# Kernel optimization log

Measured on AMD Instinct MI355X. Metric: run time of the kernel, lower is better.

The kernel has to match this reference:

```python
import jax, jax.numpy as jnp
import numpy as np

C = 64
CR = C // 16  # reduction=16 -> query/key channels
B, H, W = 2, 80, 80


def setup_inputs() -> dict:
    key = jax.random.key(0)
    ks = jax.random.split(key, 13)
    s = 0.05
    return {
        "a": jax.random.normal(ks[0], (B, C, H, W), jnp.float32),
        "b": jax.random.normal(ks[1], (B, C, H, W), jnp.float32),
        "c": jax.random.normal(ks[2], (B, C, H, W), jnp.float32),
        # attentionAB (queries from a, keys from b)
        "wq_ab": jax.random.normal(ks[3], (CR, C), jnp.float32) * s,
        "bq_ab": jax.random.normal(ks[4], (CR,), jnp.float32) * s,
        "wk_ab": jax.random.normal(ks[5], (CR, C), jnp.float32) * s,
        "bk_ab": jax.random.normal(ks[6], (CR,), jnp.float32) * s,
        # attentionBC (queries from c, keys from b)
        "wq_bc": jax.random.normal(ks[7], (CR, C), jnp.float32) * s,
        "bq_bc": jax.random.normal(ks[8], (CR,), jnp.float32) * s,
        "wk_bc": jax.random.normal(ks[9], (CR, C), jnp.float32) * s,
        "bk_bc": jax.random.normal(ks[10], (CR,), jnp.float32) * s,
        # outer value conv on b
        "wv": jax.random.normal(ks[11], (C, C), jnp.float32) * s,
        "bv": jax.random.normal(ks[12], (C,), jnp.float32) * s,
    }


def _proj(x_flat, w, bias):
    # conv1x1 on flattened [B, C, N] -> [B, D, N]
    return jnp.einsum("dc,bcn->bdn", w, x_flat) + bias[None, :, None]


def _attention(x1_flat, x2_flat, wq, bq, wk, bk):
    q = _proj(x1_flat, wq, bq)  # [B, CR, N1]
    k = _proj(x2_flat, wk, bk)  # [B, CR, N2]
    scores = jnp.einsum("bdn,bdm->bnm", q, k)  # [B, N1, N2]
    return jax.nn.softmax(scores, axis=-1)


def reference(a, b, c, wq_ab, bq_ab, wk_ab, bk_ab, wq_bc, bq_bc, wk_bc, bk_bc, wv, bv):
    bsz, ch, h, w = b.shape
    n = h * w
    af = a.reshape(bsz, ch, n)
    bf = b.reshape(bsz, ch, n)
    cf = c.reshape(bsz, ch, n)

    attn_ba = _attention(af, bf, wq_ab, bq_ab, wk_ab, bk_ab)  # [B, Na, Nb]
    attn_bc = _attention(cf, bf, wq_bc, bq_bc, wk_bc, bk_bc)  # [B, Nc, Nb]

    values_b = _proj(bf, wv, bv)  # [B, C, Nb]

    # bmm(values_b, attn^T): contract over key positions m (of b)
    enh_ba = jnp.einsum("bcm,bnm->bcn", values_b, attn_ba)
    enh_bc = jnp.einsum("bcm,bnm->bcn", values_b, attn_bc)
    enhanced = (enh_ba + enh_bc) * 0.5
    return enhanced.reshape(bsz, ch, h, w)
```

## Files before the change

kernel.cpp:

```cpp
#include <hip/hip_runtime.h>
#include <hip/hip_bf16.h>

#define NPIX 6400
#define LOG2E 1.44269504088896340736f
#define KH 4
#define KEYS 1600
#define NCH 25
#define QF 2

typedef _Float16 half_t;
typedef _Float16 half4 __attribute__((ext_vector_type(4)));
typedef float float4x __attribute__((ext_vector_type(4)));


__global__ __launch_bounds__(256) void qk_proj_kernel(
    const float* __restrict__ a, const float* __restrict__ b, const float* __restrict__ c,
    const float* __restrict__ wq_ab, const float* __restrict__ bq_ab,
    const float* __restrict__ wk_ab, const float* __restrict__ bk_ab,
    const float* __restrict__ wq_bc, const float* __restrict__ bq_bc,
    const float* __restrict__ wk_bc, const float* __restrict__ bk_bc,
    half_t* __restrict__ qp, half_t* __restrict__ kp)
{
    int tid = blockIdx.x * 256 + threadIdx.x;
    int d = tid & 3;
    int n = (tid >> 2) % NPIX;
    int bz = (tid >> 2) / NPIX;
    const float* A = a + bz * 64 * NPIX + n;
    const float* B = b + bz * 64 * NPIX + n;
    const float* C = c + bz * 64 * NPIX + n;
    float qab = 0.f, kab = 0.f, qbc = 0.f, kbc = 0.f;
#pragma unroll 4
    for (int ch = 0; ch < 64; ++ch) {
        float av = A[ch * NPIX], bv = B[ch * NPIX], cv = C[ch * NPIX];
        qab += wq_ab[d * 64 + ch] * av;
        kab += wk_ab[d * 64 + ch] * bv;
        qbc += wq_bc[d * 64 + ch] * cv;
        kbc += wk_bc[d * 64 + ch] * bv;
    }
    qp[((bz * 2 + 0) * NPIX + n) * 4 + d] = (half_t)((qab + bq_ab[d]) * LOG2E);
    qp[((bz * 2 + 1) * NPIX + n) * 4 + d] = (half_t)((qbc + bq_bc[d]) * LOG2E);
    kp[((bz * 2 + 0) * NPIX + n) * 4 + d] = (half_t)(kab + bk_ab[d]);
    kp[((bz * 2 + 1) * NPIX + n) * 4 + d] = (half_t)(kbc + bk_bc[d]);
}

__global__ __launch_bounds__(256) void v_proj_kernel(
    const float* __restrict__ b, const float* __restrict__ wv,
    const float* __restrict__ bvb, half_t* __restrict__ vp)
{
    int tid = blockIdx.x * 256 + threadIdx.x;
    int n4 = tid % 1600;
    int c  = (tid / 1600) & 63;
    int bz = tid / (1600 * 64);
    const float* B = b + bz * 64 * NPIX + n4 * 4;
    float bias = bvb[c];
    float4x acc = {bias, bias, bias, bias};
    for (int ch = 0; ch < 64; ++ch) {
        float4x bv = *(const float4x*)(B + ch * NPIX);
        float wcc = wv[c * 64 + ch];
        acc += wcc * bv;
    }
    half4 hv = {(half_t)acc[0], (half_t)acc[1], (half_t)acc[2], (half_t)acc[3]};
    *(half4*)(vp + (bz * 64 + c) * NPIX + n4 * 4) = hv;
}


__global__ __launch_bounds__(256) void attn_kernel(
    const half_t* __restrict__ qp, const half_t* __restrict__ kp,
    const half_t* __restrict__ vp, float* __restrict__ num, float* __restrict__ lsum)
{
    int bid = blockIdx.x;
    int swz = (bid & 7) * 100 + (bid >> 3);
    int qc = swz % 50;
    int br = (swz / 50) & 1;
    int bz = (swz / 100) & 1;
    int kh = swz / 200;

    int tid = threadIdx.x;
    int lane = tid & 63, w = tid >> 6;
    int g = lane >> 4, qi = lane & 15;
    int qbase = qc * 128 + w * 32;

    const half_t* Q = qp + ((bz * 2 + br) * NPIX + qbase) * 4;
    const half_t* K = kp + ((bz * 2 + br) * NPIX + kh * KEYS) * 4;
    const half_t* V = vp + bz * 64 * NPIX + kh * KEYS;

    half4 hz = {(half_t)0, (half_t)0, (half_t)0, (half_t)0};
    half4 qf[QF];
#pragma unroll
    for (int i = 0; i < QF; ++i)
        qf[i] = (lane < 16) ? *(const half4*)(Q + (i * 16 + lane) * 4) : hz;

    float4x accs[QF][4] = {{{0,0,0,0},{0,0,0,0},{0,0,0,0},{0,0,0,0}},
                           {{0,0,0,0},{0,0,0,0},{0,0,0,0},{0,0,0,0}}};
    float lrun[QF] = {0.f, 0.f};

    __shared__ char lds[2][64 * 144];
    int cc0 = tid >> 3, so0 = tid & 7;
    int cc1 = cc0 + 32;

    float4x ga = *(const float4x*)(V + cc0 * NPIX + so0 * 8);
    float4x gb = *(const float4x*)(V + cc1 * NPIX + so0 * 8);
    half4 kc[4];
#pragma unroll
    for (int t = 0; t < 4; ++t)
        kc[t] = (lane < 16) ? *(const half4*)(K + (t * 16 + lane) * 4) : hz;
    *(float4x*)(lds[0] + cc0 * 144 + so0 * 16) = ga;
    *(float4x*)(lds[0] + cc1 * 144 + so0 * 16) = gb;
    __syncthreads();

    int cur = 0;
    for (int chn = 0; chn < NCH; ++chn) {
        bool more = (chn + 1 < NCH);
        float4x gna, gnb;
        half4 kn[4];
        if (more) {
            int m0n = (chn + 1) * 64;
            gna = *(const float4x*)(V + cc0 * NPIX + m0n + so0 * 8);
            gnb = *(const float4x*)(V + cc1 * NPIX + m0n + so0 * 8);
#pragma unroll
            for (int t = 0; t < 4; ++t)
                kn[t] = (lane < 16) ? *(const half4*)(K + (m0n + t * 16 + lane) * 4) : hz;
        }
        const char* lb = lds[cur];
#pragma unroll
        for (int t = 0; t < 4; ++t) {
            half4 vf[4];
#pragma unroll
            for (int cb = 0; cb < 4; ++cb)
                vf[cb] = *(const half4*)(lb + (cb * 16 + qi) * 144 + t * 32 + g * 8);
#pragma unroll
            for (int i = 0; i < QF; ++i) {
                float4x zero = {0.f, 0.f, 0.f, 0.f};
                float4x sc = __builtin_amdgcn_mfma_f32_16x16x16f16(kc[t], qf[i], zero, 0, 0, 0);
                float p0 = exp2f(sc[0]), p1 = exp2f(sc[1]), p2 = exp2f(sc[2]), p3 = exp2f(sc[3]);
                lrun[i] += (p0 + p1) + (p2 + p3);
                half4 pf = {(half_t)p0, (half_t)p1, (half_t)p2, (half_t)p3};
#pragma unroll
                for (int cb = 0; cb < 4; ++cb)
                    accs[i][cb] = __builtin_amdgcn_mfma_f32_16x16x16f16(vf[cb], pf, accs[i][cb], 0, 0, 0);
            }
        }
        if (more) {
            *(float4x*)(lds[cur ^ 1] + cc0 * 144 + so0 * 16) = gna;
            *(float4x*)(lds[cur ^ 1] + cc1 * 144 + so0 * 16) = gnb;
#pragma unroll
            for (int t = 0; t < 4; ++t) kc[t] = kn[t];
        }
        __syncthreads();
        cur ^= 1;
    }

    float* numb = num + (bz * 2 + br) * 64 * NPIX;
#pragma unroll
    for (int i = 0; i < QF; ++i) {
        float l = lrun[i];
        l += __shfl_xor(l, 16, 64);
        l += __shfl_xor(l, 32, 64);
        int q = qbase + i * 16 + qi;
        if (g == 0) atomicAdd(&lsum[(bz * 2 + br) * NPIX + q], l);
#pragma unroll
        for (int cb = 0; cb < 4; ++cb)
#pragma unroll
            for (int r = 0; r < 4; ++r)
                atomicAdd(&numb[(cb * 16 + 4 * g + r) * NPIX + q], accs[i][cb][r]);
    }
}

__global__ __launch_bounds__(256) void norm_kernel(
    const float* __restrict__ num, const float* __restrict__ lsum, float* __restrict__ out)
{
    int tid = blockIdx.x * 256 + threadIdx.x;
    int n4 = tid % 1600;
    int c  = (tid / 1600) & 63;
    int bz = tid / (1600 * 64);
    float4x lA = *(const float4x*)(lsum + (bz * 2 + 0) * NPIX + n4 * 4);
    float4x lC = *(const float4x*)(lsum + (bz * 2 + 1) * NPIX + n4 * 4);
    float4x vA = *(const float4x*)(num + ((bz * 2 + 0) * 64 + c) * NPIX + n4 * 4);
    float4x vC = *(const float4x*)(num + ((bz * 2 + 1) * 64 + c) * NPIX + n4 * 4);
    float4x r;
#pragma unroll
    for (int j = 0; j < 4; ++j)
        r[j] = 0.5f * (vA[j] * __builtin_amdgcn_rcpf(lA[j]) +
                       vC[j] * __builtin_amdgcn_rcpf(lC[j]));
    *(float4x*)(out + (bz * 64 + c) * NPIX + n4 * 4) = r;
}

extern "C" void kernel_launch(void* const* d_in, const int* in_sizes, int n_in,
                              void* d_out, int out_size, void* d_ws, size_t ws_size,
                              hipStream_t stream) {
    (void)in_sizes; (void)n_in; (void)out_size; (void)ws_size;
    const float* a     = (const float*)d_in[0];
    const float* b     = (const float*)d_in[1];
    const float* c     = (const float*)d_in[2];
    const float* wq_ab = (const float*)d_in[3];
    const float* bq_ab = (const float*)d_in[4];
    const float* wk_ab = (const float*)d_in[5];
    const float* bk_ab = (const float*)d_in[6];
    const float* wq_bc = (const float*)d_in[7];
    const float* bq_bc = (const float*)d_in[8];
    const float* wk_bc = (const float*)d_in[9];
    const float* bk_bc = (const float*)d_in[10];
    const float* wv    = (const float*)d_in[11];
    const float* bv    = (const float*)d_in[12];
    float* out = (float*)d_out;

    half_t* qp = (half_t*)d_ws;
    half_t* kp = qp + 2 * 2 * NPIX * 4;
    half_t* vp = kp + 2 * 2 * NPIX * 4;
    float* num  = (float*)(vp + 2 * 64 * NPIX);
    float* lsum = num + 2 * 2 * 64 * NPIX;

    hipMemsetAsync(num, 0, (size_t)(2 * 2 * 64 * NPIX + 2 * 2 * NPIX) * sizeof(float), stream);

    qk_proj_kernel<<<200, 256, 0, stream>>>(a, b, c, wq_ab, bq_ab, wk_ab, bk_ab,
                                            wq_bc, bq_bc, wk_bc, bk_bc, qp, kp);
    v_proj_kernel<<<800, 256, 0, stream>>>(b, wv, bv, vp);
    attn_kernel<<<800, 256, 0, stream>>>(qp, kp, vp, num, lsum);
    norm_kernel<<<800, 256, 0, stream>>>(num, lsum, out);
}
```

Before: 213.4 us.

## Merge projection kernels, split keys five ways, and repack V LDS tiles

The QK and V projection kernels become one launch that branches on block index, and each V thread now computes two output channels. The attention kernel splits keys into 5 chunks of 1280 instead of 4 of 1600, giving 1000 blocks instead of 800 for better CU fill on the MI355X. The V staging to LDS uses 8-byte loads with a 136-byte row stride to cut bank conflicts. The cost is more atomicAdd traffic into num and lsum, since each query now gets one more partial sum.

```diff
diff --git a/kernel.cpp b/kernel.cpp
--- a/kernel.cpp
+++ b/kernel.cpp
@@ -3,73 +3,74 @@
 
 #define NPIX 6400
 #define LOG2E 1.44269504088896340736f
-#define KH 4
-#define KEYS 1600
-#define NCH 25
+#define KH 5
+#define KEYS 1280
+#define NCH 20
 #define QF 2
+#define VSTRIDE 136
 
 typedef _Float16 half_t;
 typedef _Float16 half4 __attribute__((ext_vector_type(4)));
 typedef float float4x __attribute__((ext_vector_type(4)));
-
-
-__global__ __launch_bounds__(256) void qk_proj_kernel(
+typedef unsigned long long u64;
+
+__global__ __launch_bounds__(256) void proj_kernel(
     const float* __restrict__ a, const float* __restrict__ b, const float* __restrict__ c,
     const float* __restrict__ wq_ab, const float* __restrict__ bq_ab,
     const float* __restrict__ wk_ab, const float* __restrict__ bk_ab,
     const float* __restrict__ wq_bc, const float* __restrict__ bq_bc,
     const float* __restrict__ wk_bc, const float* __restrict__ bk_bc,
-    half_t* __restrict__ qp, half_t* __restrict__ kp)
+    const float* __restrict__ wv, const float* __restrict__ bvb,
+    half_t* __restrict__ qp, half_t* __restrict__ kp, half_t* __restrict__ vp)
 {
-    int tid = blockIdx.x * 256 + threadIdx.x;
-    int d = tid & 3;
-    int n = (tid >> 2) % NPIX;
-    int bz = (tid >> 2) / NPIX;
-    const float* A = a + bz * 64 * NPIX + n;
-    const float* B = b + bz * 64 * NPIX + n;
-    const float* C = c + bz * 64 * NPIX + n;
-    float qab = 0.f, kab = 0.f, qbc = 0.f, kbc = 0.f;
+    int bid = blockIdx.x;
+    if (bid < 400) {
+        int tid = bid * 256 + threadIdx.x;
+        int n4 = tid % 1600;
+        int cc = (tid / 1600) & 31;
+        int bz = tid / (1600 * 32);
+        const float* B = b + bz * 64 * NPIX + n4 * 4;
+        float b0 = bvb[cc], b1 = bvb[cc + 32];
+        float4x acc0 = {b0, b0, b0, b0}, acc1 = {b1, b1, b1, b1};
+        for (int ch = 0; ch < 64; ++ch) {
+            float4x bv = *(const float4x*)(B + ch * NPIX);
+            acc0 += wv[cc * 64 + ch] * bv;
+            acc1 += wv[(cc + 32) * 64 + ch] * bv;
+        }
+        half4 h0 = {(half_t)acc0[0], (half_t)acc0[1], (half_t)acc0[2], (half_t)acc0[3]};
+        half4 h1 = {(half_t)acc1[0], (half_t)acc1[1], (half_t)acc1[2], (half_t)acc1[3]};
+        *(half4*)(vp + (bz * 64 + cc) * NPIX + n4 * 4) = h0;
+        *(half4*)(vp + (bz * 64 + cc + 32) * NPIX + n4 * 4) = h1;
+    } else {
+        int tid = (bid - 400) * 256 + threadIdx.x;
+        int d = tid & 3;
+        int n = (tid >> 2) % NPIX;
+        int bz = (tid >> 2) / NPIX;
+        const float* A = a + bz * 64 * NPIX + n;
+        const float* B = b + bz * 64 * NPIX + n;
+        const float* C = c + bz * 64 * NPIX + n;
+        float qab = 0.f, kab = 0.f, qbc = 0.f, kbc = 0.f;
 #pragma unroll 4
-    for (int ch = 0; ch < 64; ++ch) {
-        float av = A[ch * NPIX], bv = B[ch * NPIX], cv = C[ch * NPIX];
-        qab += wq_ab[d * 64 + ch] * av;
-        kab += wk_ab[d * 64 + ch] * bv;
-        qbc += wq_bc[d * 64 + ch] * cv;
-        kbc += wk_bc[d * 64 + ch] * bv;
-    }
-    qp[((bz * 2 + 0) * NPIX + n) * 4 + d] = (half_t)((qab + bq_ab[d]) * LOG2E);
-    qp[((bz * 2 + 1) * NPIX + n) * 4 + d] = (half_t)((qbc + bq_bc[d]) * LOG2E);
-    kp[((bz * 2 + 0) * NPIX + n) * 4 + d] = (half_t)(kab + bk_ab[d]);
-    kp[((bz * 2 + 1) * NPIX + n) * 4 + d] = (half_t)(kbc + bk_bc[d]);
-}
-
-__global__ __launch_bounds__(256) void v_proj_kernel(
-    const float* __restrict__ b, const float* __restrict__ wv,
-    const float* __restrict__ bvb, half_t* __restrict__ vp)
-{
-    int tid = blockIdx.x * 256 + threadIdx.x;
-    int n4 = tid % 1600;
-    int c  = (tid / 1600) & 63;
-    int bz = tid / (1600 * 64);
-    const float* B = b + bz * 64 * NPIX + n4 * 4;
-    float bias = bvb[c];
-    float4x acc = {bias, bias, bias, bias};
-    for (int ch = 0; ch < 64; ++ch) {
-        float4x bv = *(const float4x*)(B + ch * NPIX);
-        float wcc = wv[c * 64 + ch];
-        acc += wcc * bv;
-    }
-    half4 hv = {(half_t)acc[0], (half_t)acc[1], (half_t)acc[2], (half_t)acc[3]};
-    *(half4*)(vp + (bz * 64 + c) * NPIX + n4 * 4) = hv;
-}
-
+        for (int ch = 0; ch < 64; ++ch) {
+            float av = A[ch * NPIX], bv = B[ch * NPIX], cv = C[ch * NPIX];
+            qab += wq_ab[d * 64 + ch] * av;
+            kab += wk_ab[d * 64 + ch] * bv;
+            qbc += wq_bc[d * 64 + ch] * cv;
+            kbc += wk_bc[d * 64 + ch] * bv;
+        }
+        qp[((bz * 2 + 0) * NPIX + n) * 4 + d] = (half_t)((qab + bq_ab[d]) * LOG2E);
+        qp[((bz * 2 + 1) * NPIX + n) * 4 + d] = (half_t)((qbc + bq_bc[d]) * LOG2E);
+        kp[((bz * 2 + 0) * NPIX + n) * 4 + d] = (half_t)(kab + bk_ab[d]);
+        kp[((bz * 2 + 1) * NPIX + n) * 4 + d] = (half_t)(kbc + bk_bc[d]);
+    }
+}
 
 __global__ __launch_bounds__(256) void attn_kernel(
     const half_t* __restrict__ qp, const half_t* __restrict__ kp,
     const half_t* __restrict__ vp, float* __restrict__ num, float* __restrict__ lsum)
 {
     int bid = blockIdx.x;
-    int swz = (bid & 7) * 100 + (bid >> 3);
+    int swz = (bid & 7) * 125 + (bid >> 3);
     int qc = swz % 50;
     int br = (swz / 50) & 1;
     int bz = (swz / 100) & 1;
@@ -94,29 +95,37 @@
                            {{0,0,0,0},{0,0,0,0},{0,0,0,0},{0,0,0,0}}};
     float lrun[QF] = {0.f, 0.f};
 
-    __shared__ char lds[2][64 * 144];
-    int cc0 = tid >> 3, so0 = tid & 7;
-    int cc1 = cc0 + 32;
-
-    float4x ga = *(const float4x*)(V + cc0 * NPIX + so0 * 8);
-    float4x gb = *(const float4x*)(V + cc1 * NPIX + so0 * 8);
+    __shared__ char lds[2][64 * VSTRIDE];
+
+    u64 vpre[4];
+#pragma unroll
+    for (int p = 0; p < 4; ++p) {
+        int idx = p * 256 + tid; int row = idx >> 4, w4 = idx & 15;
+        vpre[p] = *(const u64*)(V + row * NPIX + w4 * 4);
+    }
     half4 kc[4];
 #pragma unroll
     for (int t = 0; t < 4; ++t)
         kc[t] = (lane < 16) ? *(const half4*)(K + (t * 16 + lane) * 4) : hz;
-    *(float4x*)(lds[0] + cc0 * 144 + so0 * 16) = ga;
-    *(float4x*)(lds[0] + cc1 * 144 + so0 * 16) = gb;
+#pragma unroll
+    for (int p = 0; p < 4; ++p) {
+        int idx = p * 256 + tid; int row = idx >> 4, w4 = idx & 15;
+        *(u64*)(lds[0] + row * VSTRIDE + w4 * 8) = vpre[p];
+    }
     __syncthreads();
 
     int cur = 0;
     for (int chn = 0; chn < NCH; ++chn) {
         bool more = (chn + 1 < NCH);
-        float4x gna, gnb;
+        u64 vn[4];
         half4 kn[4];
         if (more) {
             int m0n = (chn + 1) * 64;
-            gna = *(const float4x*)(V + cc0 * NPIX + m0n + so0 * 8);
-            gnb = *(const float4x*)(V + cc1 * NPIX + m0n + so0 * 8);
+#pragma unroll
+            for (int p = 0; p < 4; ++p) {
+                int idx = p * 256 + tid; int row = idx >> 4, w4 = idx & 15;
+                vn[p] = *(const u64*)(V + row * NPIX + m0n + w4 * 4);
+            }
 #pragma unroll
             for (int t = 0; t < 4; ++t)
                 kn[t] = (lane < 16) ? *(const half4*)(K + (m0n + t * 16 + lane) * 4) : hz;
@@ -127,7 +136,7 @@
             half4 vf[4];
 #pragma unroll
             for (int cb = 0; cb < 4; ++cb)
-                vf[cb] = *(const half4*)(lb + (cb * 16 + qi) * 144 + t * 32 + g * 8);
+                vf[cb] = *(const half4*)(lb + (cb * 16 + qi) * VSTRIDE + t * 32 + g * 8);
 #pragma unroll
             for (int i = 0; i < QF; ++i) {
                 float4x zero = {0.f, 0.f, 0.f, 0.f};
@@ -141,8 +150,11 @@
             }
         }
         if (more) {
-            *(float4x*)(lds[cur ^ 1] + cc0 * 144 + so0 * 16) = gna;
-            *(float4x*)(lds[cur ^ 1] + cc1 * 144 + so0 * 16) = gnb;
+#pragma unroll
+            for (int p = 0; p < 4; ++p) {
+                int idx = p * 256 + tid; int row = idx >> 4, w4 = idx & 15;
+                *(u64*)(lds[cur ^ 1] + row * VSTRIDE + w4 * 8) = vn[p];
+            }
 #pragma unroll
             for (int t = 0; t < 4; ++t) kc[t] = kn[t];
         }
@@ -212,9 +224,8 @@
 
     hipMemsetAsync(num, 0, (size_t)(2 * 2 * 64 * NPIX + 2 * 2 * NPIX) * sizeof(float), stream);
 
-    qk_proj_kernel<<<200, 256, 0, stream>>>(a, b, c, wq_ab, bq_ab, wk_ab, bk_ab,
-                                            wq_bc, bq_bc, wk_bc, bk_bc, qp, kp);
-    v_proj_kernel<<<800, 256, 0, stream>>>(b, wv, bv, vp);
-    attn_kernel<<<800, 256, 0, stream>>>(qp, kp, vp, num, lsum);
+    proj_kernel<<<600, 256, 0, stream>>>(a, b, c, wq_ab, bq_ab, wk_ab, bk_ab,
+                                         wq_bc, bq_bc, wk_bc, bk_bc, wv, bv, qp, kp, vp);
+    attn_kernel<<<1000, 256, 0, stream>>>(qp, kp, vp, num, lsum);
     norm_kernel<<<800, 256, 0, stream>>>(num, lsum, out);
 }
```

New measurement: 199.5 us. 6.5% less time.
